# Optimization experiments

Hardware: AMD Instinct MI355X
Metric: run time of the kernel (lower is better)

## Reference

```python
import jax, jax.numpy as jnp
import numpy as np

C, H, L, P = 256, 8, 4, 4   # embed_dim, num_heads, num_levels, num_points
B, N = 2, 16384             # batch, total queries
SHAPES = [(64, 64), (128, 128), (256, 256), (512, 512)]  # last = base (finest)


def setup_inputs() -> dict:
    key = jax.random.key(0)
    ks = jax.random.split(key, 16)
    d = {}
    d["query"] = jax.random.normal(ks[0], (N, C), jnp.float32)
    d["query_offsets"] = jnp.array([0, N // 2], jnp.int32)
    base_h, base_w = SHAPES[-1]
    # un-normalized reference points in finest-level pixel coords, kept away from edges
    d["reference_points"] = (
        jax.random.uniform(ks[1], (N, 2), jnp.float32)
        * jnp.array([base_h - 16, base_w - 16], jnp.float32) + 8.0
    )
    for l, (h, w) in enumerate(SHAPES):
        d[f"value{l}"] = jax.random.normal(ks[2 + l], (B, h, w, C), jnp.float32) * 0.1
    d["W_off"] = jax.random.normal(ks[6], (C, H * L * P * 2), jnp.float32) * 0.01
    d["b_off"] = jax.random.normal(ks[7], (H * L * P * 2,), jnp.float32) * 2.0
    d["W_attn"] = jax.random.normal(ks[8], (C, H * L * P), jnp.float32) * 0.02
    d["b_attn"] = jnp.zeros((H * L * P,), jnp.float32)
    d["W_val"] = jax.random.normal(ks[9], (C, C), jnp.float32) * (1.0 / np.sqrt(C))
    d["b_val"] = jnp.zeros((C,), jnp.float32)
    d["W_out"] = jax.random.normal(ks[10], (C, C), jnp.float32) * (1.0 / np.sqrt(C))
    d["b_out"] = jnp.zeros((C,), jnp.float32)
    return d


def _bilinear_sample(v, loc, batch_id):
    """v: [B,h,w,H,dh] per-head feature map; loc: [N,H,P,2] (i,j) pixel coords;
    batch_id: [N]. Returns [N,H,P,dh]. Mirrors sparse_interp: shift by 0.5,
    clamp_min 0, floor, frac weights, max-index clamp."""
    h, w = v.shape[1], v.shape[2]
    sc = jnp.maximum(loc - 0.5, 0.0)
    i0 = jnp.floor(sc).astype(jnp.int32)
    frac = sc - jnp.floor(sc)
    b = batch_id[:, None, None]                 # [N,1,1]
    hidx = jnp.arange(H)[None, :, None]         # [1,H,1]

    def g(di, dj):
        ii = jnp.clip(i0[..., 0] + di, 0, h - 1)
        jj = jnp.clip(i0[..., 1] + dj, 0, w - 1)
        return v[b, ii, jj, hidx]               # [N,H,P,dh]

    dw = frac[..., 0:1]  # down weight
    rw = frac[..., 1:2]  # right weight
    uw, lw = 1.0 - dw, 1.0 - rw
    return uw * lw * g(0, 0) + uw * rw * g(0, 1) + dw * lw * g(1, 0) + dw * rw * g(1, 1)


def reference(query, query_offsets, reference_points, value0, value1, value2, value3,
              W_off, b_off, W_attn, b_attn, W_val, b_val, W_out, b_out):
    values = [value0, value1, value2, value3]
    n = query.shape[0]
    dh = C // H
    # sampling offsets and attention weights from query
    off = (query @ W_off + b_off).reshape(n, H, L, P, 2)
    attn = jax.nn.softmax((query @ W_attn + b_attn).reshape(n, H, L * P), axis=-1)
    attn = attn.reshape(n, H, L, P)
    base = jnp.asarray(values[-1].shape[1:3], jnp.float32)
    # which batch element each query belongs to
    batch_id = jnp.searchsorted(query_offsets, jnp.arange(n), side="right") - 1
    sampled = []
    for l, v in enumerate(values):
        hl, wl = v.shape[1], v.shape[2]
        scaler = jnp.array([hl, wl], jnp.float32) / base
        loc = (reference_points[:, None, None, :] + off[:, :, l]) * scaler  # [N,H,P,2]
        # value_proj: per-pixel 1x1 linear, then split heads
        vp = (v @ W_val + b_val).reshape(v.shape[0], hl, wl, H, dh)
        sampled.append(_bilinear_sample(vp, loc, batch_id))
    sampled = jnp.stack(sampled, axis=2)        # [N,H,L,P,dh]
    out = (sampled * attn[..., None]).sum(axis=(2, 3)).reshape(n, C)
    return out @ W_out + b_out
```

## Files before the change

kernel.cpp:

```cpp
#include <hip/hip_runtime.h>


typedef float f32x4 __attribute__((ext_vector_type(4)));
typedef _Float16 f16;
typedef f16 f16x8 __attribute__((ext_vector_type(8)));
typedef f16 f16x4 __attribute__((ext_vector_type(4)));

template<int M>
__global__ __launch_bounds__(M)
void gemm_rb(const float* __restrict__ X, const float* __restrict__ W,
             const float* __restrict__ bias, float* __restrict__ Y) {
    __shared__ float xt[32 * 256];
    const int tid = threadIdx.x;
    const long row0 = (long)blockIdx.x * 32;
    const float4* src = (const float4*)(X + row0 * 256);
    float4* dst4 = (float4*)xt;
    for (int i = tid; i < 32 * 64; i += M) dst4[i] = src[i];
    __syncthreads();

    constexpr int CG = M / 4;
    const int cg = tid % CG, qg = tid / CG;
    const int c0 = cg * 4, q0 = qg * 8;

    f32x4 acc[8];
#pragma unroll
    for (int qi = 0; qi < 8; ++qi) acc[qi] = (f32x4){0.f, 0.f, 0.f, 0.f};

    for (int k4 = 0; k4 < 64; ++k4) {
        f32x4 w[4];
#pragma unroll
        for (int r = 0; r < 4; ++r)
            w[r] = *(const f32x4*)&W[(size_t)(k4 * 4 + r) * M + c0];
        f32x4 xv[8];
#pragma unroll
        for (int qi = 0; qi < 8; ++qi)
            xv[qi] = *(const f32x4*)&xt[(q0 + qi) * 256 + k4 * 4];
#pragma unroll
        for (int qi = 0; qi < 8; ++qi) {
            f32x4 a = acc[qi];
            const f32x4 x = xv[qi];
            a.x = fmaf(x.x, w[0].x, a.x); a.y = fmaf(x.x, w[0].y, a.y);
            a.z = fmaf(x.x, w[0].z, a.z); a.w = fmaf(x.x, w[0].w, a.w);
            a.x = fmaf(x.y, w[1].x, a.x); a.y = fmaf(x.y, w[1].y, a.y);
            a.z = fmaf(x.y, w[1].z, a.z); a.w = fmaf(x.y, w[1].w, a.w);
            a.x = fmaf(x.z, w[2].x, a.x); a.y = fmaf(x.z, w[2].y, a.y);
            a.z = fmaf(x.z, w[2].z, a.z); a.w = fmaf(x.z, w[2].w, a.w);
            a.x = fmaf(x.w, w[3].x, a.x); a.y = fmaf(x.w, w[3].y, a.y);
            a.z = fmaf(x.w, w[3].z, a.z); a.w = fmaf(x.w, w[3].w, a.w);
            acc[qi] = a;
        }
    }

    const f32x4 bv = *(const f32x4*)&bias[c0];
#pragma unroll
    for (int qi = 0; qi < 8; ++qi) {
        f32x4 o = acc[qi];
        o.x += bv.x; o.y += bv.y; o.z += bv.z; o.w += bv.w;
        *(f32x4*)&Y[(size_t)(row0 + q0 + qi) * M + c0] = o;
    }
}

__global__ __launch_bounds__(384)
void gemm_qproj(const float* __restrict__ X,
                const float* __restrict__ W_off, const float* __restrict__ b_off,
                const float* __restrict__ W_attn, const float* __restrict__ b_attn,
                float* __restrict__ Y1, float* __restrict__ Y2) {
    __shared__ float xt[32 * 260];
    const int tid = threadIdx.x;
    const long row0 = (long)blockIdx.x * 32;
    const float4* src = (const float4*)(X + row0 * 256);
    for (int i = tid; i < 32 * 64; i += 384) {
        const int r = i >> 6, c4 = i & 63;
        *(float4*)(xt + r * 260 + c4 * 4) = src[i];
    }
    __syncthreads();

    const int cg = tid % 96, qg = tid / 96;
    const int c0 = cg * 4, q0 = qg * 8;
    const bool off_part = (c0 < 256);
    const float* Wp = off_part ? (W_off + c0) : (W_attn + (c0 - 256));
    const float* bp = off_part ? (b_off + c0) : (b_attn + (c0 - 256));
    const int ldW = off_part ? 256 : 128;
    float* Yp = off_part ? (Y1 + c0) : (Y2 + (c0 - 256));

    f32x4 acc[8];
#pragma unroll
    for (int qi = 0; qi < 8; ++qi) acc[qi] = (f32x4){0.f, 0.f, 0.f, 0.f};

    for (int k4 = 0; k4 < 64; ++k4) {
        f32x4 w[4];
#pragma unroll
        for (int r = 0; r < 4; ++r)
            w[r] = *(const f32x4*)&Wp[(size_t)(k4 * 4 + r) * ldW];
        f32x4 xv[8];
#pragma unroll
        for (int qi = 0; qi < 8; ++qi)
            xv[qi] = *(const f32x4*)&xt[(q0 + qi) * 260 + k4 * 4];
#pragma unroll
        for (int qi = 0; qi < 8; ++qi) {
            f32x4 a = acc[qi];
            const f32x4 x = xv[qi];
            a.x = fmaf(x.x, w[0].x, a.x); a.y = fmaf(x.x, w[0].y, a.y);
            a.z = fmaf(x.x, w[0].z, a.z); a.w = fmaf(x.x, w[0].w, a.w);
            a.x = fmaf(x.y, w[1].x, a.x); a.y = fmaf(x.y, w[1].y, a.y);
            a.z = fmaf(x.y, w[1].z, a.z); a.w = fmaf(x.y, w[1].w, a.w);
            a.x = fmaf(x.z, w[2].x, a.x); a.y = fmaf(x.z, w[2].y, a.y);
            a.z = fmaf(x.z, w[2].z, a.z); a.w = fmaf(x.z, w[2].w, a.w);
            a.x = fmaf(x.w, w[3].x, a.x); a.y = fmaf(x.w, w[3].y, a.y);
            a.z = fmaf(x.w, w[3].z, a.z); a.w = fmaf(x.w, w[3].w, a.w);
            acc[qi] = a;
        }
    }

    const f32x4 bv = *(const f32x4*)bp;
#pragma unroll
    for (int qi = 0; qi < 8; ++qi) {
        f32x4 o = acc[qi];
        o.x += bv.x; o.y += bv.y; o.z += bv.z; o.w += bv.w;
        *(f32x4*)&Yp[(size_t)(row0 + q0 + qi) * ldW] = o;
    }
}

#define NBINS 4096

__device__ __forceinline__ int bin_of(float ri, float rj) {
    int bi = (int)ri >> 3, bj = (int)rj >> 3;
    bi = min(63, max(0, bi)); bj = min(63, max(0, bj));
    return bi * 64 + bj;
}

__global__ void bin_hist(const float* __restrict__ refp, int* __restrict__ hist, int N) {
    const int n = blockIdx.x * blockDim.x + threadIdx.x;
    if (n < N) atomicAdd(&hist[bin_of(refp[2 * n], refp[2 * n + 1])], 1);
}

__global__ __launch_bounds__(256)
void bin_scan(const int* __restrict__ hist, int* __restrict__ binptr) {
    __shared__ int part[256];
    const int t = threadIdx.x;
    int vals[16], excl[16], run = 0;
#pragma unroll
    for (int i = 0; i < 16; ++i) { vals[i] = hist[t * 16 + i]; }
#pragma unroll
    for (int i = 0; i < 16; ++i) { excl[i] = run; run += vals[i]; }
    part[t] = run;
    __syncthreads();
    int off = 0;
    for (int i = 0; i < t; ++i) off += part[i];
#pragma unroll
    for (int i = 0; i < 16; ++i) binptr[t * 16 + i] = off + excl[i];
}

__global__ void bin_scatter(const float* __restrict__ refp, int* __restrict__ binptr,
                            int* __restrict__ perm, int N) {
    const int n = blockIdx.x * blockDim.x + threadIdx.x;
    if (n < N) {
        const int b = bin_of(refp[2 * n], refp[2 * n + 1]);
        const int pos = atomicAdd(&binptr[b], 1);
        perm[pos] = n;
    }
}

__global__ __launch_bounds__(256)
void prep_wvF(const float* __restrict__ W, f16* __restrict__ wvF) {
    const int k = blockIdx.x, n = threadIdx.x;
    const int ks = k >> 5, kg = (k >> 3) & 3, j = k & 7;
    const int tile = n >> 4, l15 = n & 15;
    const int lane = (kg << 4) | l15;
    wvF[((size_t)(ks * 16 + tile) * 512) + lane * 8 + j] = (f16)W[(size_t)k * 256 + n];
}

__global__ __launch_bounds__(256)
void proj_val_all(const float* __restrict__ v0, const float* __restrict__ v1,
                  const float* __restrict__ v2, const float* __restrict__ v3,
                  const f16* __restrict__ wvF, const float* __restrict__ bval,
                  f16* __restrict__ vp0, f16* __restrict__ vp1,
                  f16* __restrict__ vp2, f16* __restrict__ vp3) {
    __shared__ f16 At[32][264];
    const int tid = threadIdx.x;

    const int bid = blockIdx.x;
    const float* V; f16* VP; long px0; long hwsq;
    if (bid < 256)        { V = v0; VP = vp0; px0 = (long)bid * 32;          hwsq = 4096;   }
    else if (bid < 1280)  { V = v1; VP = vp1; px0 = (long)(bid - 256) * 32;  hwsq = 16384;  }
    else if (bid < 5376)  { V = v2; VP = vp2; px0 = (long)(bid - 1280) * 32; hwsq = 65536;  }
    else                  { V = v3; VP = vp3; px0 = (long)(bid - 5376) * 32; hwsq = 262144; }

    {
        const int wv_ = tid >> 6, ln_ = tid & 63;
#pragma unroll
        for (int i = 0; i < 8; ++i) {
            const int px = wv_ + i * 4;
            const float4 v4 = *(const float4*)(V + (px0 + px) * 256 + ln_ * 4);
            f16x4 h4 = {(f16)v4.x, (f16)v4.y, (f16)v4.z, (f16)v4.w};
            *(f16x4*)(&At[px][ln_ * 4]) = h4;
        }
    }
    __syncthreads();

    const int wave = tid >> 6, lane = tid & 63;
    const int l15 = lane & 15, kg = lane >> 4;

    f32x4 acc[2][4];
#pragma unroll
    for (int a = 0; a < 2; ++a)
#pragma unroll
        for (int b = 0; b < 4; ++b) acc[a][b] = (f32x4){0.f, 0.f, 0.f, 0.f};

#pragma unroll
    for (int ks = 0; ks < 8; ++ks) {
        f16x8 wf[4];
#pragma unroll
        for (int ct = 0; ct < 4; ++ct)
            wf[ct] = *(const f16x8*)(wvF + ((size_t)(ks * 16 + wave * 4 + ct) * 512) + lane * 8);
        f16x8 vf[2];
#pragma unroll
        for (int pt = 0; pt < 2; ++pt)
            vf[pt] = *(const f16x8*)(&At[pt * 16 + l15][ks * 32 + kg * 8]);
#pragma unroll
        for (int pt = 0; pt < 2; ++pt)
#pragma unroll
            for (int ct = 0; ct < 4; ++ct)
                acc[pt][ct] = __builtin_amdgcn_mfma_f32_16x16x32_f16(wf[ct], vf[pt], acc[pt][ct], 0, 0, 0);
    }

    __syncthreads();

    const int ch0 = wave * 64;
#pragma unroll
    for (int ct = 0; ct < 4; ++ct) {
        const int chb = ch0 + ct * 16 + kg * 4;
        const float4 bv = *(const float4*)(bval + chb);
#pragma unroll
        for (int pt = 0; pt < 2; ++pt) {
            f16x4 o = {(f16)(acc[pt][ct].x + bv.x), (f16)(acc[pt][ct].y + bv.y),
                       (f16)(acc[pt][ct].z + bv.z), (f16)(acc[pt][ct].w + bv.w)};
            *(f16x4*)(&At[pt * 16 + l15][chb]) = o;
        }
    }
    __syncthreads();

    const long bt = (px0 >= hwsq) ? 1 : 0;
    const long pxb = px0 - bt * hwsq;
    f16* base = VP + (size_t)bt * hwsq * 256;
#pragma unroll
    for (int i = 0; i < 4; ++i) {
        const int c2 = i * 256 + tid;
        const int hh = c2 >> 7;
        const int rem = c2 & 127;
        const int px = rem >> 2;
        const int sub = rem & 3;
        *(f16x8*)(base + (size_t)hh * hwsq * 32 + (pxb + px) * 32 + sub * 8) =
            *(const f16x8*)(&At[px][hh * 32 + sub * 8]);
    }
}

#define GQPB 4
__global__ __launch_bounds__(256)
void gather_vp(const float* __restrict__ offs_all,
               const float* __restrict__ logits_all,
               const float* __restrict__ refpts,
               const int* __restrict__ qoff, int n_off,
               const int* __restrict__ perm,
               const f16* __restrict__ vp0, const f16* __restrict__ vp1,
               const f16* __restrict__ vp2, const f16* __restrict__ vp3,
               float* __restrict__ val_out) {
    __shared__ float sOff[GQPB][256];
    __shared__ float sAttn[GQPB][128];
    __shared__ int   sQ[GQPB];
    const int tid = threadIdx.x;

    const int bid = blockIdx.x;
    const int cpx = gridDim.x >> 3;
    const int swz = (bid & 7) * cpx + (bid >> 3);
    const int n0p = swz * GQPB;

    if (tid < GQPB) sQ[tid] = perm[n0p + tid];
    __syncthreads();

    {
        const int q = tid >> 6, i = tid & 63;
        const int nq = sQ[q];
        ((f32x4*)sOff[q])[i] = ((const f32x4*)(offs_all + (size_t)nq * 256))[i];
        if (i < 32) ((f32x4*)sAttn[q])[i] = ((const f32x4*)(logits_all + (size_t)nq * 128))[i];
    }
    __syncthreads();

    if (tid < GQPB * 8) {
        float* row = &sAttn[tid >> 3][(tid & 7) * 16];
        float m = -1e30f;
#pragma unroll
        for (int i = 0; i < 16; ++i) m = fmaxf(m, row[i]);
        float s = 0.f;
#pragma unroll
        for (int i = 0; i < 16; ++i) { const float e = expf(row[i] - m); row[i] = e; s += e; }
        const float inv = 1.f / s;
#pragma unroll
        for (int i = 0; i < 16; ++i) row[i] *= inv;
    }
    __syncthreads();

    const int q = tid >> 6, h = (tid >> 3) & 7;
    const int l8 = tid & 7, s = l8 & 3, jc = l8 >> 2;
    const int n = sQ[q];
    int b = 0;
    for (int i = 1; i < n_off; ++i) if (n >= qoff[i]) b = i;
    const float ri = refpts[2 * n], rj = refpts[2 * n + 1];
    const int s8 = s * 8;

    float acc[8];
#pragma unroll
    for (int j = 0; j < 8; ++j) acc[j] = 0.f;

#pragma unroll
    for (int l = 0; l < 4; ++l) {
        const int hw = (l == 0 ? 64 : (l == 1 ? 128 : (l == 2 ? 256 : 512)));
        const long hwsq = (long)hw * hw;
        const float sc = (float)hw * (1.0f / 512.0f);
        const f16* vbl = (l == 0 ? vp0 : (l == 1 ? vp1 : (l == 2 ? vp2 : vp3)));
        const f16* __restrict__ vb = vbl + (size_t)b * hwsq * 256 + (size_t)h * hwsq * 32 + s8;

        int   a0[4], a1[4];
        float w0v[4], w1v[4];
#pragma unroll
        for (int p = 0; p < 4; ++p) {
            const int oi = ((h * 4 + l) * 4 + p) * 2;
            const float fi = (ri + sOff[q][oi]) * sc;
            const float fj = (rj + sOff[q][oi + 1]) * sc;
            const float a = sAttn[q][(h * 4 + l) * 4 + p];
            const float sci = fmaxf(fi - 0.5f, 0.f);
            const float scj = fmaxf(fj - 0.5f, 0.f);
            const float fl_i = floorf(sci), fl_j = floorf(scj);
            const int i0 = (int)fl_i, j0 = (int)fl_j;
            const float fri = sci - fl_i, frj = scj - fl_j;
            const int i0c = min(i0, hw - 1), i1c = min(i0 + 1, hw - 1);
            const int j0c = min(j0, hw - 1), j1c = min(j0 + 1, hw - 1);
            const float uw = 1.f - fri, lw = 1.f - frj;
            const int jsel = jc ? j1c : j0c;
            a0[p] = (i0c * hw + jsel) * 32;
            a1[p] = (i1c * hw + jsel) * 32;
            w0v[p] = (jc ? uw * frj : uw * lw) * a;
            w1v[p] = (jc ? fri * frj : fri * lw) * a;
        }

        f16x8 buf[8];
#pragma unroll
        for (int p = 0; p < 4; ++p) {
            buf[2 * p]     = *(const f16x8*)(vb + (size_t)a0[p]);
            buf[2 * p + 1] = *(const f16x8*)(vb + (size_t)a1[p]);
        }
        asm volatile("" : "+v"(buf[0]), "+v"(buf[1]), "+v"(buf[2]), "+v"(buf[3]),
                          "+v"(buf[4]), "+v"(buf[5]), "+v"(buf[6]), "+v"(buf[7])
                        :: "memory");
#pragma unroll
        for (int p = 0; p < 4; ++p) {
            const float wa = w0v[p], wb = w1v[p];
#pragma unroll
            for (int j = 0; j < 8; ++j) {
                acc[j] = fmaf(wa, (float)buf[2 * p][j], acc[j]);
                acc[j] = fmaf(wb, (float)buf[2 * p + 1][j], acc[j]);
            }
        }
    }

#pragma unroll
    for (int j = 0; j < 8; ++j) acc[j] += __shfl_xor(acc[j], 4);

    if (jc == 0) {
        float* op = val_out + (size_t)n * 256 + h * 32 + s8;
        *(f32x4*)op       = (f32x4){acc[0], acc[1], acc[2], acc[3]};
        *(f32x4*)(op + 4) = (f32x4){acc[4], acc[5], acc[6], acc[7]};
    }
}

extern "C" void kernel_launch(void* const* d_in, const int* in_sizes, int n_in,
                              void* d_out, int out_size, void* d_ws, size_t ws_size,
                              hipStream_t stream) {
    const float* query  = (const float*)d_in[0];
    const int*   qoff   = (const int*)d_in[1];
    const float* refp   = (const float*)d_in[2];
    const float* v0     = (const float*)d_in[3];
    const float* v1     = (const float*)d_in[4];
    const float* v2     = (const float*)d_in[5];
    const float* v3     = (const float*)d_in[6];
    const float* W_off  = (const float*)d_in[7];
    const float* b_off  = (const float*)d_in[8];
    const float* W_attn = (const float*)d_in[9];
    const float* b_attn = (const float*)d_in[10];
    const float* W_val  = (const float*)d_in[11];
    const float* b_val  = (const float*)d_in[12];
    const float* W_out  = (const float*)d_in[13];
    const float* b_out  = (const float*)d_in[14];
    float* out = (float*)d_out;

    const int N = in_sizes[0] / 256;
    const int n_off = in_sizes[1];

    float* P1off  = (float*)d_ws;
    float* P1attn = P1off + (size_t)N * 256;
    int*   hist   = (int*)(P1attn + (size_t)N * 128);
    int*   binptr = hist + NBINS;
    int*   perm   = binptr + NBINS;

    const int M0 = 2 * 64 * 64, M1 = 2 * 128 * 128, M2 = 2 * 256 * 256, M3 = 2 * 512 * 512;
    const size_t base_b = (size_t)N * 256 * 4 + (size_t)N * 128 * 4 + (size_t)(2 * NBINS + N) * 4;

    hipMemsetAsync(hist, 0, NBINS * sizeof(int), stream);
    bin_hist<<<(N + 255) / 256, 256, 0, stream>>>(refp, hist, N);
    bin_scan<<<1, 256, 0, stream>>>(hist, binptr);
    bin_scatter<<<(N + 255) / 256, 256, 0, stream>>>(refp, binptr, perm, N);

    gemm_qproj<<<N / 32, 384, 0, stream>>>(query, W_off, b_off, W_attn, b_attn,
                                           P1off, P1attn);

    f16* wvF = (f16*)((char*)d_ws + base_b);
    f16* vp0 = wvF + 65536;
    f16* vp1 = vp0 + (size_t)M0 * 256;
    f16* vp2 = vp1 + (size_t)M1 * 256;
    f16* vp3 = vp2 + (size_t)M2 * 256;

    prep_wvF<<<256, 256, 0, stream>>>(W_val, wvF);
    proj_val_all<<<21760, 256, 0, stream>>>(v0, v1, v2, v3, wvF, b_val,
                                            vp0, vp1, vp2, vp3);

    gather_vp<<<N / GQPB, 256, 0, stream>>>(P1off, P1attn, refp, qoff, n_off,
                                            perm, vp0, vp1, vp2, vp3, out);

    gemm_rb<256><<<N / 32, 256, 0, stream>>>(out, W_out, b_out, out);
}
```

Baseline: 463.1 us.

## Make value projection persistent with register-prefetched next tile

Turns the value-projection kernel into a persistent grid-stride loop over 2048 blocks. Each block prefetches the next tile's fp32 input into registers while it runs the MFMA work on the current tile, so load latency overlaps with compute. The output is now written directly from the accumulators to the head-major layout rather than staged through shared memory, which drops a barrier and a copy. In exchange the 8-byte global stores are less coalesced, register pressure rises, and with fewer blocks there may be less latency hiding than before.

```diff
diff --git a/kernel.cpp b/kernel.cpp
--- a/kernel.cpp
+++ b/kernel.cpp
@@ -170,89 +170,103 @@
     wvF[((size_t)(ks * 16 + tile) * 512) + lane * 8 + j] = (f16)W[(size_t)k * 256 + n];
 }
 
+#define NT_PROJ 21760
 __global__ __launch_bounds__(256)
-void proj_val_all(const float* __restrict__ v0, const float* __restrict__ v1,
-                  const float* __restrict__ v2, const float* __restrict__ v3,
-                  const f16* __restrict__ wvF, const float* __restrict__ bval,
-                  f16* __restrict__ vp0, f16* __restrict__ vp1,
-                  f16* __restrict__ vp2, f16* __restrict__ vp3) {
+void proj_val_pipe(const float* __restrict__ v0, const float* __restrict__ v1,
+                   const float* __restrict__ v2, const float* __restrict__ v3,
+                   const f16* __restrict__ wvF, const float* __restrict__ bval,
+                   f16* __restrict__ vp0, f16* __restrict__ vp1,
+                   f16* __restrict__ vp2, f16* __restrict__ vp3) {
     __shared__ f16 At[32][264];
     const int tid = threadIdx.x;
-
-    const int bid = blockIdx.x;
-    const float* V; f16* VP; long px0; long hwsq;
-    if (bid < 256)        { V = v0; VP = vp0; px0 = (long)bid * 32;          hwsq = 4096;   }
-    else if (bid < 1280)  { V = v1; VP = vp1; px0 = (long)(bid - 256) * 32;  hwsq = 16384;  }
-    else if (bid < 5376)  { V = v2; VP = vp2; px0 = (long)(bid - 1280) * 32; hwsq = 65536;  }
-    else                  { V = v3; VP = vp3; px0 = (long)(bid - 5376) * 32; hwsq = 262144; }
-
-    {
-        const int wv_ = tid >> 6, ln_ = tid & 63;
-#pragma unroll
-        for (int i = 0; i < 8; ++i) {
-            const int px = wv_ + i * 4;
-            const float4 v4 = *(const float4*)(V + (px0 + px) * 256 + ln_ * 4);
-            f16x4 h4 = {(f16)v4.x, (f16)v4.y, (f16)v4.z, (f16)v4.w};
-            *(f16x4*)(&At[px][ln_ * 4]) = h4;
-        }
-    }
-    __syncthreads();
-
     const int wave = tid >> 6, lane = tid & 63;
     const int l15 = lane & 15, kg = lane >> 4;
-
-    f32x4 acc[2][4];
-#pragma unroll
-    for (int a = 0; a < 2; ++a)
-#pragma unroll
-        for (int b = 0; b < 4; ++b) acc[a][b] = (f32x4){0.f, 0.f, 0.f, 0.f};
-
-#pragma unroll
-    for (int ks = 0; ks < 8; ++ks) {
-        f16x8 wf[4];
-#pragma unroll
-        for (int ct = 0; ct < 4; ++ct)
-            wf[ct] = *(const f16x8*)(wvF + ((size_t)(ks * 16 + wave * 4 + ct) * 512) + lane * 8);
-        f16x8 vf[2];
-#pragma unroll
-        for (int pt = 0; pt < 2; ++pt)
-            vf[pt] = *(const f16x8*)(&At[pt * 16 + l15][ks * 32 + kg * 8]);
-#pragma unroll
-        for (int pt = 0; pt < 2; ++pt)
+    const int G = gridDim.x;
+
+#define TILE_INFO(T, V, VP, PX0, HWSQ) do {                                    \
+    if ((T) < 256)        { V = v0; VP = vp0; PX0 = (long)(T) * 32;          HWSQ = 4096;   } \
+    else if ((T) < 1280)  { V = v1; VP = vp1; PX0 = (long)((T) - 256) * 32;  HWSQ = 16384;  } \
+    else if ((T) < 5376)  { V = v2; VP = vp2; PX0 = (long)((T) - 1280) * 32; HWSQ = 65536;  } \
+    else                  { V = v3; VP = vp3; PX0 = (long)((T) - 5376) * 32; HWSQ = 262144; } \
+} while (0)
+
+    int t = blockIdx.x;
+    if (t >= NT_PROJ) return;
+
+    float4 st[8];
+    {
+        const float* V; f16* VP; long px0, hwsq;
+        TILE_INFO(t, V, VP, px0, hwsq);
+#pragma unroll
+        for (int i = 0; i < 8; ++i)
+            st[i] = *(const float4*)(V + (px0 + wave + i * 4) * 256 + lane * 4);
+    }
+
+    for (; t < NT_PROJ; t += G) {
+        __syncthreads();
+#pragma unroll
+        for (int i = 0; i < 8; ++i) {
+            const int px = wave + i * 4;
+            f16x4 h4 = {(f16)st[i].x, (f16)st[i].y, (f16)st[i].z, (f16)st[i].w};
+            *(f16x4*)(&At[px][lane * 4]) = h4;
+        }
+        __syncthreads();
+
+        const int tn = t + G;
+        if (tn < NT_PROJ) {
+            const float* Vn; f16* VPn; long px0n, hwsqn;
+            TILE_INFO(tn, Vn, VPn, px0n, hwsqn);
+#pragma unroll
+            for (int i = 0; i < 8; ++i)
+                st[i] = *(const float4*)(Vn + (px0n + wave + i * 4) * 256 + lane * 4);
+            asm volatile("" ::: "memory");
+        }
+
+        f32x4 acc[2][4];
+#pragma unroll
+        for (int a = 0; a < 2; ++a)
+#pragma unroll
+            for (int b = 0; b < 4; ++b) acc[a][b] = (f32x4){0.f, 0.f, 0.f, 0.f};
+
+#pragma unroll
+        for (int ks = 0; ks < 8; ++ks) {
+            f16x8 wf[4];
 #pragma unroll
             for (int ct = 0; ct < 4; ++ct)
-                acc[pt][ct] = __builtin_amdgcn_mfma_f32_16x16x32_f16(wf[ct], vf[pt], acc[pt][ct], 0, 0, 0);
-    }
-
-    __syncthreads();
-
-    const int ch0 = wave * 64;
-#pragma unroll
-    for (int ct = 0; ct < 4; ++ct) {
-        const int chb = ch0 + ct * 16 + kg * 4;
-        const float4 bv = *(const float4*)(bval + chb);
-#pragma unroll
-        for (int pt = 0; pt < 2; ++pt) {
-            f16x4 o = {(f16)(acc[pt][ct].x + bv.x), (f16)(acc[pt][ct].y + bv.y),
-                       (f16)(acc[pt][ct].z + bv.z), (f16)(acc[pt][ct].w + bv.w)};
-            *(f16x4*)(&At[pt * 16 + l15][chb]) = o;
-        }
-    }
-    __syncthreads();
-
-    const long bt = (px0 >= hwsq) ? 1 : 0;
-    const long pxb = px0 - bt * hwsq;
-    f16* base = VP + (size_t)bt * hwsq * 256;
-#pragma unroll
-    for (int i = 0; i < 4; ++i) {
-        const int c2 = i * 256 + tid;
-        const int hh = c2 >> 7;
-        const int rem = c2 & 127;
-        const int px = rem >> 2;
-        const int sub = rem & 3;
-        *(f16x8*)(base + (size_t)hh * hwsq * 32 + (pxb + px) * 32 + sub * 8) =
-            *(const f16x8*)(&At[px][hh * 32 + sub * 8]);
-    }
+                wf[ct] = *(const f16x8*)(wvF + ((size_t)(ks * 16 + wave * 4 + ct) * 512) + lane * 8);
+            f16x8 vf[2];
+#pragma unroll
+            for (int pt = 0; pt < 2; ++pt)
+                vf[pt] = *(const f16x8*)(&At[pt * 16 + l15][ks * 32 + kg * 8]);
+#pragma unroll
+            for (int pt = 0; pt < 2; ++pt)
+#pragma unroll
+                for (int ct = 0; ct < 4; ++ct)
+                    acc[pt][ct] = __builtin_amdgcn_mfma_f32_16x16x32_f16(wf[ct], vf[pt], acc[pt][ct], 0, 0, 0);
+        }
+
+        {
+            const float* Vc; f16* VP; long px0, hwsq;
+            TILE_INFO(t, Vc, VP, px0, hwsq);
+            const long bt = (px0 >= hwsq) ? 1 : 0;
+            const long pxb = px0 - bt * hwsq;
+            f16* base = VP + (size_t)bt * hwsq * 256;
+#pragma unroll
+            for (int ct = 0; ct < 4; ++ct) {
+                const int chb = wave * 64 + ct * 16 + kg * 4;
+                const int hh = chb >> 5, co = chb & 31;
+                const float4 bv = *(const float4*)(bval + chb);
+#pragma unroll
+                for (int pt = 0; pt < 2; ++pt) {
+                    f16x4 o = {(f16)(acc[pt][ct].x + bv.x), (f16)(acc[pt][ct].y + bv.y),
+                               (f16)(acc[pt][ct].z + bv.z), (f16)(acc[pt][ct].w + bv.w)};
+                    *(f16x4*)(base + (size_t)hh * hwsq * 32 +
+                              (size_t)(pxb + pt * 16 + l15) * 32 + co) = o;
+                }
+            }
+        }
+    }
+#undef TILE_INFO
 }
 
 #define GQPB 4
@@ -420,7 +434,7 @@
     f16* vp3 = vp2 + (size_t)M2 * 256;
 
     prep_wvF<<<256, 256, 0, stream>>>(W_val, wvF);
-    proj_val_all<<<21760, 256, 0, stream>>>(v0, v1, v2, v3, wvF, b_val,
+    proj_val_pipe<<<2048, 256, 0, stream>>>(v0, v1, v2, v3, wvF, b_val,
                                             vp0, vp1, vp2, vp3);
 
     gather_vp<<<N / GQPB, 256, 0, stream>>>(P1off, P1attn, refp, qoff, n_off,
```

Measured after the change: 461.8 us. No clear change (-0.3%).
